# Performance work log

Hardware: AMD Instinct MI355X
Metric: run time of the kernel (lower is better)

## Reference

```python
import jax, jax.numpy as jnp
import numpy as np

B = 4096
MAX_ATOMS = 2048


def setup_inputs() -> dict:
    key = jax.random.key(0)
    k1, k2, k3 = jax.random.split(key, 3)
    coords_input = jax.random.normal(k1, (B, 3 * MAX_ATOMS), dtype=jnp.float32) * 10.0
    coords_target = jax.random.normal(k2, (B, 3 * MAX_ATOMS), dtype=jnp.float32) * 10.0
    num_atoms = jax.random.randint(k3, (B,), 64, MAX_ATOMS + 1, dtype=jnp.int32)
    return {"coords_input": coords_input, "coords_target": coords_target, "num_atoms": num_atoms}


def _kabsch_rmsd(coords_input, coords_target, num_atoms):
    b, f = coords_input.shape
    n_max = f // 3
    x = coords_input.reshape(b, n_max, 3)   # [B, N, 3] interleaved xyz per atom
    y = coords_target.reshape(b, n_max, 3)
    mask = (jnp.arange(n_max)[None, :] < num_atoms[:, None])[..., None]  # [B, N, 1]
    n = num_atoms.astype(x.dtype)[:, None, None]                          # [B, 1, 1]

    # masked centroids, then center and zero out padded atoms
    xm = jnp.where(mask, x, 0.0)
    ym = jnp.where(mask, y, 0.0)
    xc = (x - xm.sum(axis=1, keepdims=True) / n) * mask
    yc = (y - ym.sum(axis=1, keepdims=True) / n) * mask

    # 3x3 cross-covariance per batch element
    C = jnp.einsum('bni,bnj->bij', xc, yc)  # [B, 3, 3]
    s = jnp.linalg.svd(C, compute_uv=False)  # singular values, descending [B, 3]
    # Kabsch determinant correction: d = sign(det(U) det(V)) = sign(det(C))
    d = jnp.where(jnp.linalg.det(C) < 0.0, -1.0, 1.0).astype(x.dtype)
    trace = s[:, 0] + s[:, 1] + d * s[:, 2]

    gx = jnp.sum(xc * xc, axis=(1, 2))
    gy = jnp.sum(yc * yc, axis=(1, 2))
    msd = (gx + gy - 2.0 * trace) / jnp.squeeze(n, (1, 2))
    return jnp.sqrt(jnp.maximum(msd, 0.0))


def reference(coords_input, coords_target, num_atoms):
    return _kabsch_rmsd(coords_input, coords_target, num_atoms)
```

## Files before the change

kernel.cpp:

```cpp
#include <hip/hip_runtime.h>
#include <math.h>

#define N_MAX 2048
#define SEG 4
#define SEG_ATOMS 512
#define SEG_QUADS 128

#define ACC_ATOM(X0,X1,X2,Y0,Y1,Y2,M) do {                          \
    const float m_ = (M);                                           \
    const float x0 = (X0)*m_, x1 = (X1)*m_, x2 = (X2)*m_;           \
    const float y0 = (Y0)*m_, y1 = (Y1)*m_, y2 = (Y2)*m_;           \
    acc[0]  += x0;    acc[1]  += x1;    acc[2]  += x2;              \
    acc[3]  += y0;    acc[4]  += y1;    acc[5]  += y2;              \
    acc[6]  += x0*y0; acc[7]  += x0*y1; acc[8]  += x0*y2;           \
    acc[9]  += x1*y0; acc[10] += x1*y1; acc[11] += x1*y2;           \
    acc[12] += x2*y0; acc[13] += x2*y1; acc[14] += x2*y2;           \
    acc[15] += x0*x0 + x1*x1 + x2*x2;                               \
    acc[16] += y0*y0 + y1*y1 + y2*y2;                               \
} while (0)

#define ACC_QUAD(Q) do {                                            \
    const int a0 = 4 * (Q);                                         \
    const int fi = 3 * (Q);                                         \
    const float4 xa = x4[fi + 0], xb = x4[fi + 1], xc = x4[fi + 2]; \
    const float4 ya = y4[fi + 0], yb = y4[fi + 1], yc = y4[fi + 2]; \
    const float m1 = (a0 + 1 < n) ? 1.0f : 0.0f;                    \
    const float m2 = (a0 + 2 < n) ? 1.0f : 0.0f;                    \
    const float m3 = (a0 + 3 < n) ? 1.0f : 0.0f;                    \
    ACC_ATOM(xa.x, xa.y, xa.z, ya.x, ya.y, ya.z, 1.0f);             \
    ACC_ATOM(xa.w, xb.x, xb.y, ya.w, yb.x, yb.y, m1);               \
    ACC_ATOM(xb.z, xb.w, xc.x, yb.z, yb.w, yc.x, m2);               \
    ACC_ATOM(xc.y, xc.z, xc.w, yc.y, yc.z, yc.w, m3);               \
} while (0)

__global__ __launch_bounds__(256) void kabsch_sums_kernel(
    const float* __restrict__ X, const float* __restrict__ Y,
    const int* __restrict__ num_atoms, float* __restrict__ ws, int B)
{
    const int wave = threadIdx.x >> 6;
    const int lane = threadIdx.x & 63;
    const int gw   = blockIdx.x * 4 + wave;
    const int b    = gw >> 2;
    const int s    = gw & 3;
    const int n    = num_atoms[b];
    if (s * SEG_ATOMS >= n) return;

    const int nq = (n + 3) >> 2;
    const float4* __restrict__ x4 =
        reinterpret_cast<const float4*>(X + (size_t)b * (3 * N_MAX));
    const float4* __restrict__ y4 =
        reinterpret_cast<const float4*>(Y + (size_t)b * (3 * N_MAX));

    float acc[17];
#pragma unroll
    for (int i = 0; i < 17; ++i) acc[i] = 0.0f;

    const int q0 = s * SEG_QUADS + lane;
    if (q0 < nq)      ACC_QUAD(q0);
    const int q1 = q0 + 64;
    if (q1 < nq)      ACC_QUAD(q1);

#pragma unroll
    for (int i = 0; i < 17; ++i) {
#pragma unroll
        for (int off = 32; off > 0; off >>= 1)
            acc[i] += __shfl_down(acc[i], off);
    }

    if (lane == 0) {
#pragma unroll
        for (int i = 0; i < 17; ++i)
            ws[(size_t)(s * 17 + i) * B + b] = acc[i];
    }
}

__global__ __launch_bounds__(256) void kabsch_epilogue_kernel(
    const float* __restrict__ ws, const int* __restrict__ num_atoms,
    float* __restrict__ out, int B)
{
    const int b = blockIdx.x * 256 + threadIdx.x;
    if (b >= B) return;

    const int n    = num_atoms[b];
    const int nseg = (n + SEG_ATOMS - 1) >> 9;

    double s[17];
#pragma unroll
    for (int i = 0; i < 17; ++i) s[i] = 0.0;
    for (int h = 0; h < nseg; ++h) {
#pragma unroll
        for (int i = 0; i < 17; ++i)
            s[i] += (double)ws[(size_t)(h * 17 + i) * B + b];
    }

    const double dn = (double)n;
    const double Sx0 = s[0], Sx1 = s[1], Sx2 = s[2];
    const double Sy0 = s[3], Sy1 = s[4], Sy2 = s[5];

    double C[3][3];
    C[0][0] = s[6]  - Sx0 * Sy0 / dn;
    C[0][1] = s[7]  - Sx0 * Sy1 / dn;
    C[0][2] = s[8]  - Sx0 * Sy2 / dn;
    C[1][0] = s[9]  - Sx1 * Sy0 / dn;
    C[1][1] = s[10] - Sx1 * Sy1 / dn;
    C[1][2] = s[11] - Sx1 * Sy2 / dn;
    C[2][0] = s[12] - Sx2 * Sy0 / dn;
    C[2][1] = s[13] - Sx2 * Sy1 / dn;
    C[2][2] = s[14] - Sx2 * Sy2 / dn;

    const double gx = s[15] - (Sx0*Sx0 + Sx1*Sx1 + Sx2*Sx2) / dn;
    const double gy = s[16] - (Sy0*Sy0 + Sy1*Sy1 + Sy2*Sy2) / dn;

    const double det =
        C[0][0] * (C[1][1]*C[2][2] - C[1][2]*C[2][1]) -
        C[0][1] * (C[1][0]*C[2][2] - C[1][2]*C[2][0]) +
        C[0][2] * (C[1][0]*C[2][1] - C[1][1]*C[2][0]);

    double A00 = C[0][0]*C[0][0] + C[1][0]*C[1][0] + C[2][0]*C[2][0];
    double A11 = C[0][1]*C[0][1] + C[1][1]*C[1][1] + C[2][1]*C[2][1];
    double A22 = C[0][2]*C[0][2] + C[1][2]*C[1][2] + C[2][2]*C[2][2];
    double A01 = C[0][0]*C[0][1] + C[1][0]*C[1][1] + C[2][0]*C[2][1];
    double A02 = C[0][0]*C[0][2] + C[1][0]*C[1][2] + C[2][0]*C[2][2];
    double A12 = C[0][1]*C[0][2] + C[1][1]*C[1][2] + C[2][1]*C[2][2];

    double e0, e1, e2;
    const double q  = (A00 + A11 + A22) / 3.0;
    const double p1 = A01*A01 + A02*A02 + A12*A12;
    const double p2 = (A00-q)*(A00-q) + (A11-q)*(A11-q) + (A22-q)*(A22-q)
                      + 2.0 * p1;
    if (p2 <= 0.0) {
        e0 = e1 = e2 = q;
    } else {
        const double p = sqrt(p2 / 6.0);
        const double ip = 1.0 / p;
        const double b00 = (A00 - q) * ip, b11 = (A11 - q) * ip,
                     b22 = (A22 - q) * ip;
        const double b01 = A01 * ip, b02 = A02 * ip, b12 = A12 * ip;
        double r = 0.5 * (b00 * (b11*b22 - b12*b12)
                        - b01 * (b01*b22 - b12*b02)
                        + b02 * (b01*b12 - b11*b02));
        r = fmin(1.0, fmax(-1.0, r));
        const double phi = acos(r) / 3.0;
        e0 = q + 2.0 * p * cos(phi);
        e2 = q + 2.0 * p * cos(phi + 2.0943951023931953);
        e1 = 3.0 * q - e0 - e2;
    }

    const double s0 = sqrt(fmax(e0, 0.0));
    const double s1 = sqrt(fmax(e1, 0.0));
    const double s2 = sqrt(fmax(e2, 0.0));
    const double dsign = (det < 0.0) ? -1.0 : 1.0;
    const double trace = s0 + s1 + dsign * s2;

    const double msd = (gx + gy - 2.0 * trace) / dn;
    out[b] = (float)sqrt(fmax(msd, 0.0));
}

extern "C" void kernel_launch(void* const* d_in, const int* in_sizes, int n_in,
                              void* d_out, int out_size, void* d_ws, size_t ws_size,
                              hipStream_t stream) {
    const float* coords_input  = (const float*)d_in[0];
    const float* coords_target = (const float*)d_in[1];
    const int*   num_atoms     = (const int*)d_in[2];
    float* out = (float*)d_out;
    float* ws  = (float*)d_ws;

    const int B = out_size;
    const int blocksA = B * SEG / 4;
    kabsch_sums_kernel<<<blocksA, 256, 0, stream>>>(coords_input, coords_target,
                                                    num_atoms, ws, B);
    const int blocksB = (B + 255) / 256;
    kabsch_epilogue_kernel<<<blocksB, 256, 0, stream>>>(ws, num_atoms, out, B);
}
```

Before: 201.5 us.

## Fuse sums and epilogue kernels using atomics and last-block-done counter

Merges the per-segment reduction kernel and the epilogue kernel into one launch. Segment partial sums are accumulated with float atomics into a workspace, and a per-batch counter identifies the last wave, which then runs the double-precision SVD epilogue. Batches with a single segment skip the atomics entirely. This removes one kernel launch and the workspace round trip, but adds a memset, atomics, fences, and a nondeterministic float summation order.

```diff
diff --git a/kernel.cpp b/kernel.cpp
--- a/kernel.cpp
+++ b/kernel.cpp
@@ -33,65 +33,12 @@
     ACC_ATOM(xc.y, xc.z, xc.w, yc.y, yc.z, yc.w, m3);               \
 } while (0)
 
-__global__ __launch_bounds__(256) void kabsch_sums_kernel(
-    const float* __restrict__ X, const float* __restrict__ Y,
-    const int* __restrict__ num_atoms, float* __restrict__ ws, int B)
+__device__ __forceinline__ void kabsch_epilogue(const float* sf, int n,
+                                                float* __restrict__ out, int b)
 {
-    const int wave = threadIdx.x >> 6;
-    const int lane = threadIdx.x & 63;
-    const int gw   = blockIdx.x * 4 + wave;
-    const int b    = gw >> 2;
-    const int s    = gw & 3;
-    const int n    = num_atoms[b];
-    if (s * SEG_ATOMS >= n) return;
-
-    const int nq = (n + 3) >> 2;
-    const float4* __restrict__ x4 =
-        reinterpret_cast<const float4*>(X + (size_t)b * (3 * N_MAX));
-    const float4* __restrict__ y4 =
-        reinterpret_cast<const float4*>(Y + (size_t)b * (3 * N_MAX));
-
-    float acc[17];
-#pragma unroll
-    for (int i = 0; i < 17; ++i) acc[i] = 0.0f;
-
-    const int q0 = s * SEG_QUADS + lane;
-    if (q0 < nq)      ACC_QUAD(q0);
-    const int q1 = q0 + 64;
-    if (q1 < nq)      ACC_QUAD(q1);
-
-#pragma unroll
-    for (int i = 0; i < 17; ++i) {
-#pragma unroll
-        for (int off = 32; off > 0; off >>= 1)
-            acc[i] += __shfl_down(acc[i], off);
-    }
-
-    if (lane == 0) {
-#pragma unroll
-        for (int i = 0; i < 17; ++i)
-            ws[(size_t)(s * 17 + i) * B + b] = acc[i];
-    }
-}
-
-__global__ __launch_bounds__(256) void kabsch_epilogue_kernel(
-    const float* __restrict__ ws, const int* __restrict__ num_atoms,
-    float* __restrict__ out, int B)
-{
-    const int b = blockIdx.x * 256 + threadIdx.x;
-    if (b >= B) return;
-
-    const int n    = num_atoms[b];
-    const int nseg = (n + SEG_ATOMS - 1) >> 9;
-
     double s[17];
 #pragma unroll
-    for (int i = 0; i < 17; ++i) s[i] = 0.0;
-    for (int h = 0; h < nseg; ++h) {
-#pragma unroll
-        for (int i = 0; i < 17; ++i)
-            s[i] += (double)ws[(size_t)(h * 17 + i) * B + b];
-    }
+    for (int i = 0; i < 17; ++i) s[i] = (double)sf[i];
 
     const double dn = (double)n;
     const double Sx0 = s[0], Sx1 = s[1], Sx2 = s[2];
@@ -156,6 +103,77 @@
     out[b] = (float)sqrt(fmax(msd, 0.0));
 }
 
+__global__ __launch_bounds__(256, 4) void kabsch_fused_kernel(
+    const float* __restrict__ X, const float* __restrict__ Y,
+    const int* __restrict__ num_atoms, float* __restrict__ sums,
+    int* __restrict__ cnt, float* __restrict__ out, int B)
+{
+    const int wave = threadIdx.x >> 6;
+    const int lane = threadIdx.x & 63;
+    const int gw   = blockIdx.x * 4 + wave;
+    const int b    = gw >> 2;
+    const int s    = gw & 3;
+    const int n    = num_atoms[b];
+    const int nseg = (n + SEG_ATOMS - 1) >> 9;
+    if (s >= nseg) return;
+
+    const int nq = (n + 3) >> 2;
+    const float4* __restrict__ x4 =
+        reinterpret_cast<const float4*>(X + (size_t)b * (3 * N_MAX));
+    const float4* __restrict__ y4 =
+        reinterpret_cast<const float4*>(Y + (size_t)b * (3 * N_MAX));
+
+    float acc[17];
+#pragma unroll
+    for (int i = 0; i < 17; ++i) acc[i] = 0.0f;
+
+    const int q0 = s * SEG_QUADS + lane;
+    if (q0 < nq)      ACC_QUAD(q0);
+    const int q1 = q0 + 64;
+    if (q1 < nq)      ACC_QUAD(q1);
+
+#pragma unroll
+    for (int i = 0; i < 17; ++i) {
+#pragma unroll
+        for (int off = 32; off > 0; off >>= 1)
+            acc[i] += __shfl_down(acc[i], off);
+    }
+
+    if (nseg == 1) {
+        if (lane == 0) kabsch_epilogue(acc, n, out, b);
+        return;
+    }
+
+    float myv = 0.0f;
+#pragma unroll
+    for (int i = 0; i < 17; ++i) {
+        const float t = __shfl(acc[i], 0);
+        if (lane == i) myv = t;
+    }
+    if (lane < 17) atomicAdd(&sums[(size_t)lane * B + b], myv);
+
+    __threadfence();
+
+    int last = 0;
+    if (lane == 0) {
+        const int old = atomicAdd(&cnt[b], 1);
+        last = (old == nseg - 1);
+    }
+    last = __shfl(last, 0);
+    if (!last) return;
+
+    __threadfence();
+
+    float sv = 0.0f;
+    if (lane < 17) sv = atomicAdd(&sums[(size_t)lane * B + b], 0.0f);
+
+    float sf[17];
+#pragma unroll
+    for (int i = 0; i < 17; ++i) sf[i] = __shfl(sv, i);
+
+    if (lane == 0) kabsch_epilogue(sf, n, out, b);
+}
+
 extern "C" void kernel_launch(void* const* d_in, const int* in_sizes, int n_in,
                               void* d_out, int out_size, void* d_ws, size_t ws_size,
                               hipStream_t stream) {
@@ -163,12 +181,15 @@
     const float* coords_target = (const float*)d_in[1];
     const int*   num_atoms     = (const int*)d_in[2];
     float* out = (float*)d_out;
-    float* ws  = (float*)d_ws;
 
     const int B = out_size;
+    float* sums = (float*)d_ws;
+    int*   cnt  = (int*)((char*)d_ws + (size_t)17 * B * sizeof(float));
+
+    hipMemsetAsync(d_ws, 0, (size_t)17 * B * sizeof(float) + B * sizeof(int),
+                   stream);
+
     const int blocksA = B * SEG / 4;
-    kabsch_sums_kernel<<<blocksA, 256, 0, stream>>>(coords_input, coords_target,
-                                                    num_atoms, ws, B);
-    const int blocksB = (B + 255) / 256;
-    kabsch_epilogue_kernel<<<blocksB, 256, 0, stream>>>(ws, num_atoms, out, B);
+    kabsch_fused_kernel<<<blocksA, 256, 0, stream>>>(
+        coords_input, coords_target, num_atoms, sums, cnt, out, B);
 }
```

Result: slower. 654.2 us (+224.7%).
